# Optimization experiments

Hardware: AMD Instinct MI355X
Metric: run time of the kernel (lower is better)

The kernel has to match this reference:

```python
import jax, jax.numpy as jnp
import numpy as np
from jax import lax

N_STATES = 512
VOCAB = 32000
BATCH = 16
SEQ_LEN = 128


def setup_inputs() -> dict:
    key = jax.random.key(0)
    k_ids, k_em, k_tm, k_p = jax.random.split(key, 4)
    input_ids = jax.random.randint(k_ids, (BATCH, SEQ_LEN), 0, VOCAB, dtype=jnp.int64)
    em = jax.random.normal(k_em, (N_STATES, VOCAB), dtype=jnp.float32)
    tm = jax.random.normal(k_tm, (N_STATES, N_STATES), dtype=jnp.float32)
    p = jax.random.normal(k_p, (N_STATES,), dtype=jnp.float32)
    return {"input_ids": input_ids, "em": em, "tm": tm, "p": p}


def reference(input_ids, em, tm, p):
    """HMM forward algorithm in log space; returns mean NLL (scalar).

    em: [S, V] emission logits, tm: [S, S] transition logits, p: [S] prior logits.
    do_log_softmax=True -> normalize each in log space first.
    """
    log_em = jax.nn.log_softmax(em, axis=-1)   # [S, V]
    log_tm = jax.nn.log_softmax(tm, axis=-1)   # [S, S] rows = source state
    log_p = jax.nn.log_softmax(p, axis=-1)     # [S]

    # Gather emission log-probs per token: [B, T, S]
    em_tok = log_em.T[input_ids]

    # alpha_0[b, s] = log_p[s] + log_em[s, x_0]
    alpha0 = log_p[None, :] + em_tok[:, 0]     # [B, S]

    def step(alpha, e_t):
        # alpha: [B, S_src]; log-matmul: logsumexp over source states
        a = jax.nn.logsumexp(alpha[:, :, None] + log_tm[None, :, :], axis=1) + e_t
        return a, None

    em_rest = jnp.swapaxes(em_tok[:, 1:], 0, 1)  # [T-1, B, S]
    alpha_T, _ = lax.scan(step, alpha0, em_rest)

    # loss = -mean_b log p(x_b) = -mean_b logsumexp_s alpha_T[b, s]
    loss = -jnp.mean(jax.nn.logsumexp(alpha_T, axis=-1))
    return loss
```

## Files before the change

### kernel.cpp

```cpp
#include <hip/hip_runtime.h>
#include <hip/hip_bf16.h>

#define NS 512
#define NV 32000
#define NB 16
#define NT 128

#ifndef __has_builtin
#define __has_builtin(x) 0
#endif

typedef int v8i __attribute__((ext_vector_type(8)));
typedef float v4f __attribute__((ext_vector_type(4)));

__device__ inline unsigned enc_e4m3(float x) {
    x = fminf(x, 448.0f);
    unsigned u = __float_as_uint(x);
    if (x < 0.015625f) {
        return (unsigned)(int)rintf(x * 512.0f);
    }
    unsigned u2 = u + 0x7FFFFu + ((u >> 20) & 1u);
    return (((u2 >> 23) - 120u) << 3) | ((u2 >> 20) & 7u);
}

__device__ inline unsigned pack4_e4m3(float a, float b, float c, float d) {
#if __has_builtin(__builtin_amdgcn_cvt_pk_fp8_f32)
    int v = __builtin_amdgcn_cvt_pk_fp8_f32(a, b, 0, false);
    v = __builtin_amdgcn_cvt_pk_fp8_f32(c, d, v, true);
    return (unsigned)v;
#else
    return enc_e4m3(a) | (enc_e4m3(b) << 8) | (enc_e4m3(c) << 16) | (enc_e4m3(d) << 24);
#endif
}

#define DPPMAX(x, ctrl) \
    x = fmaxf(x, __int_as_float(__builtin_amdgcn_mov_dpp(__float_as_int(x), ctrl, 0xF, 0xF, true)))
#define DPPADD(x, ctrl) \
    x = x + __int_as_float(__builtin_amdgcn_mov_dpp(__float_as_int(x), ctrl, 0xF, 0xF, true))

__global__ __launch_bounds__(256) void k_emtok_T(
    const float* __restrict__ em, const int* __restrict__ ids,
    float* __restrict__ em_lin_T)
{
    const int s   = blockIdx.x;
    const int tid = threadIdx.x;
    const float* row = em + (size_t)s * NV;

    int idv[8];
#pragma unroll
    for (int k = 0; k < 8; ++k) idv[k] = ids[tid + 256 * k];
    float g[8];
#pragma unroll
    for (int k = 0; k < 8; ++k) g[k] = row[idv[k]];

    float sum = 0.f;
    const float4* row4 = (const float4*)row;
#pragma unroll 4
    for (int i = 0; i < 31; ++i) {
        float4 v = row4[tid + 256 * i];
        sum += __expf(v.x) + __expf(v.y) + __expf(v.z) + __expf(v.w);
    }
    sum += __expf(row[31744 + tid]);

#pragma unroll
    for (int off = 32; off; off >>= 1) sum += __shfl_down(sum, off);
    __shared__ float red[4];
    __shared__ float s_scale;
    if ((tid & 63) == 0) red[tid >> 6] = sum;
    __syncthreads();
    if (tid == 0) s_scale = (1.0f / ((red[0] + red[1]) + (red[2] + red[3]))) * 0x1p-18f;
    __syncthreads();
    const float scale = s_scale;

#pragma unroll
    for (int k = 0; k < 8; ++k)
        em_lin_T[(size_t)s * (NB * NT) + tid + 256 * k] = __expf(g[k]) * scale;
}

__global__ __launch_bounds__(256) void k_tr(
    const float* __restrict__ emT, float* __restrict__ em_lin)
{
    __shared__ float tile[32][33];
    const int jb = blockIdx.x * 32;
    const int sb = blockIdx.y * 32;
    const int cc = threadIdx.x & 31;
    const int rr = threadIdx.x >> 5;
#pragma unroll
    for (int i = 0; i < 4; ++i) {
        int r = rr + 8 * i;
        tile[r][cc] = emT[(size_t)(sb + r) * (NB * NT) + jb + cc];
    }
    __syncthreads();
#pragma unroll
    for (int i = 0; i < 4; ++i) {
        int r = rr + 8 * i;
        em_lin[(size_t)(jb + r) * NS + sb + cc] = tile[cc][r];
    }
}

__global__ __launch_bounds__(64) void k_z(
    const float* __restrict__ tm, float* __restrict__ zscale)
{
    const int k    = blockIdx.x;
    const int lane = threadIdx.x;
    const float* row = tm + (size_t)k * NS;

    float4 a = ((const float4*)row)[lane * 2];
    float4 b = ((const float4*)row)[lane * 2 + 1];
    float sum = ((__expf(a.x) + __expf(a.y)) + (__expf(a.z) + __expf(a.w)))
              + ((__expf(b.x) + __expf(b.y)) + (__expf(b.z) + __expf(b.w)));
#pragma unroll
    for (int off = 32; off; off >>= 1) sum += __shfl_down(sum, off);
    if (lane == 0) zscale[k] = 1024.0f / sum;
}

__global__ __launch_bounds__(256) void k_pt2(
    const float* __restrict__ tm, const float* __restrict__ zscale,
    unsigned char* __restrict__ PT)
{
    __shared__ float tile[64][65];
    __shared__ float zs[64];
    const int kb  = blockIdx.x * 64;
    const int db  = blockIdx.y * 64;
    const int tid = threadIdx.x;
    const int c   = tid & 63;
    const int r0  = tid >> 6;

    if (tid < 64) zs[tid] = zscale[kb + tid];
#pragma unroll
    for (int i = 0; i < 16; ++i) {
        int r = r0 + 4 * i;
        tile[r][c] = tm[(size_t)(kb + r) * NS + db + c];
    }
    __syncthreads();

    const int d  = tid >> 2;
    const int ks = (tid & 3) * 16;
    unsigned px[4];
#pragma unroll
    for (int gq = 0; gq < 4; ++gq) {
        int k0 = ks + gq * 4;
        px[gq] = pack4_e4m3(__expf(tile[k0 + 0][d]) * zs[k0 + 0],
                            __expf(tile[k0 + 1][d]) * zs[k0 + 1],
                            __expf(tile[k0 + 2][d]) * zs[k0 + 2],
                            __expf(tile[k0 + 3][d]) * zs[k0 + 3]);
    }
    uint4 o; o.x = px[0]; o.y = px[1]; o.z = px[2]; o.w = px[3];
    *(uint4*)(PT + (size_t)(db + d) * NS + kb + ks) = o;
}

__global__ __launch_bounds__(512, 2) void k_scan(
    const float* __restrict__ em_lin, const unsigned char* __restrict__ PT,
    const float* __restrict__ p, float* __restrict__ out)
{
    const int bb  = blockIdx.x;
    const int tid = threadIdx.x;
    const int w   = tid >> 6;
    const int l   = tid & 63;
    const int lc  = l & 15;
    const int lq  = l >> 4;

    __shared__ unsigned Ew[16 * 128];
    __shared__ unsigned wmE[8][4];
    __shared__ unsigned mbuf[4];
    __shared__ float    wm2[8][4];
    __shared__ float    sbuf[4];

    v8i B[4][4];
#pragma unroll
    for (int nt = 0; nt < 4; ++nt) {
#pragma unroll
        for (int kt = 0; kt < 4; ++kt) {
            const uint4* src = (const uint4*)(PT + (size_t)((w * 4 + nt) * 16 + lc) * NS + kt * 128 + lq * 32);
            uint4 lo = src[0], hi = src[1];
            v8i bb8;
            bb8[0] = (int)lo.x; bb8[1] = (int)lo.y; bb8[2] = (int)lo.z; bb8[3] = (int)lo.w;
            bb8[4] = (int)hi.x; bb8[5] = (int)hi.y; bb8[6] = (int)hi.z; bb8[7] = (int)hi.w;
            B[nt][kt] = bb8;
        }
    }

    float zp = 0.f;
#pragma unroll
    for (int i = 0; i < 8; ++i) zp += __expf(p[l * 8 + i]);
    DPPADD(zp, 0x128); DPPADD(zp, 0x124); DPPADD(zp, 0xB1); DPPADD(zp, 0x4E);
    float Zp = __int_as_float(__builtin_amdgcn_readlane(__float_as_int(zp), 0))
             + __int_as_float(__builtin_amdgcn_readlane(__float_as_int(zp), 16))
             + __int_as_float(__builtin_amdgcn_readlane(__float_as_int(zp), 32))
             + __int_as_float(__builtin_amdgcn_readlane(__float_as_int(zp), 48));
    const float invZp = 1.0f / Zp;

    const int dbase0 = w * 64 + lc;
    const int gb     = bb * 4 + lq;

    const float* epb0 = em_lin + (size_t)gb * (NT * NS) + dbase0;
    float alpha[4];
#pragma unroll
    for (int nt = 0; nt < 4; ++nt)
        alpha[nt] = __expf(p[dbase0 + 16 * nt]) * invZp * epb0[16 * nt];

    int gsum = 18;
    const unsigned sel1 = (l & 1) ? 0x07030501u : 0x02060004u;
    const unsigned sel2 = (l & 2) ? 0x07060302u : 0x01000504u;
    const int mrow = 4 * lq + (l & 3);

    int aidx[8];
#pragma unroll
    for (int kt = 0; kt < 4; ++kt) {
#pragma unroll
        for (int c = 0; c < 2; ++c)
            aidx[kt * 2 + c] = lc * 32 + (((kt * 8 + lq * 2 + c) ^ lc) & 31);
    }
    int widx[4];
#pragma unroll
    for (int nt = 0; nt < 4; ++nt)
        widx[nt] = mrow * 128 + ((((w * 4 + nt) ^ mrow) & 31) << 2) + (lc >> 2);

    const float* epb = epb0 + NS;

    for (int t = 1; t < NT; ++t) {
        float epf[4];
#pragma unroll
        for (int nt = 0; nt < 4; ++nt) epf[nt] = epb[16 * nt];
        epb += NS;

        float mx = fmaxf(fmaxf(alpha[0], alpha[1]), fmaxf(alpha[2], alpha[3]));
        DPPMAX(mx, 0x128); DPPMAX(mx, 0x124); DPPMAX(mx, 0xB1); DPPMAX(mx, 0x4E);
        if (lc == 0) wmE[w][lq] = __float_as_uint(mx) >> 23;
        __syncthreads();

        if (tid < 4) {
            unsigned e0 = wmE[0][tid], e1 = wmE[1][tid], e2 = wmE[2][tid], e3 = wmE[3][tid];
            unsigned e4 = wmE[4][tid], e5 = wmE[5][tid], e6 = wmE[6][tid], e7 = wmE[7][tid];
            unsigned m01 = e0 > e1 ? e0 : e1,  m23 = e2 > e3 ? e2 : e3;
            unsigned m45 = e4 > e5 ? e4 : e5,  m67 = e6 > e7 ? e6 : e7;
            unsigned ma = m01 > m23 ? m01 : m23, mb = m45 > m67 ? m45 : m67;
            mbuf[tid] = ma > mb ? ma : mb;
        }
        __syncthreads();

        const unsigned eb = mbuf[lq];
        const float sc = __uint_as_float((261u - eb) << 23);
        gsum += (int)eb - 126;

#pragma unroll
        for (int nt = 0; nt < 4; ++nt) {
            unsigned dw = pack4_e4m3(alpha[nt] * sc, 0.f, 0.f, 0.f);
            int tmp = __builtin_amdgcn_mov_dpp((int)dw, 0xB1, 0xF, 0xF, true);
            dw = __builtin_amdgcn_perm(dw, (unsigned)tmp, sel1);
            tmp = __builtin_amdgcn_mov_dpp((int)dw, 0x4E, 0xF, 0xF, true);
            dw = __builtin_amdgcn_perm(dw, (unsigned)tmp, sel2);
            Ew[widx[nt]] = dw;
        }
        __syncthreads();

        v8i A[4];
        const uint4* eb4 = (const uint4*)&Ew[0];
#pragma unroll
        for (int kt = 0; kt < 4; ++kt) {
            uint4 lo = eb4[aidx[kt * 2 + 0]];
            uint4 hi = eb4[aidx[kt * 2 + 1]];
            v8i aa;
            aa[0] = (int)lo.x; aa[1] = (int)lo.y; aa[2] = (int)lo.z; aa[3] = (int)lo.w;
            aa[4] = (int)hi.x; aa[5] = (int)hi.y; aa[6] = (int)hi.z; aa[7] = (int)hi.w;
            A[kt] = aa;
        }

        v4f C[4];
#pragma unroll
        for (int nt = 0; nt < 4; ++nt) { C[nt][0] = 0.f; C[nt][1] = 0.f; C[nt][2] = 0.f; C[nt][3] = 0.f; }
#pragma unroll
        for (int kt = 0; kt < 4; ++kt)
#pragma unroll
            for (int nt = 0; nt < 4; ++nt)
                C[nt] = __builtin_amdgcn_mfma_scale_f32_16x16x128_f8f6f4(
                            A[kt], B[nt][kt], C[nt], 0, 0, 0, 0x7F7F7F7F, 0, 0x7F7F7F7F);

#pragma unroll
        for (int nt = 0; nt < 4; ++nt)
            alpha[nt] = C[nt][0] * epf[nt];
    }

    {
        float sm = (alpha[0] + alpha[1]) + (alpha[2] + alpha[3]);
        DPPADD(sm, 0x128); DPPADD(sm, 0x124); DPPADD(sm, 0xB1); DPPADD(sm, 0x4E);
        if (lc == 0) wm2[w][lq] = sm;
        if (w == 0 && lc == 0) sbuf[lq] = (float)gsum;
    }
    __syncthreads();
    if (tid < 4) {
        float s8 = ((wm2[0][tid] + wm2[1][tid]) + (wm2[2][tid] + wm2[3][tid]))
                 + ((wm2[4][tid] + wm2[5][tid]) + (wm2[6][tid] + wm2[7][tid]));
        float L2 = __log2f(s8) + sbuf[tid];
        atomicAdd(out, -(0.693147180559945f / 16.0f) * L2);
    }
}

extern "C" void kernel_launch(void* const* d_in, const int* in_sizes, int n_in,
                              void* d_out, int out_size, void* d_ws, size_t ws_size,
                              hipStream_t stream)
{
    const int*   ids = (const int*)d_in[0];
    const float* em  = (const float*)d_in[1];
    const float* tm  = (const float*)d_in[2];
    const float* p   = (const float*)d_in[3];
    float* out = (float*)d_out;

    float*          em_lin = (float*)d_ws;
    unsigned char*  PT     = (unsigned char*)d_ws + ((size_t)4 << 20);
    float*          zscale = (float*)((unsigned char*)d_ws + ((size_t)4 << 20) + ((size_t)256 << 10));
    float*          emT    = (float*)((unsigned char*)d_ws + ((size_t)4 << 20) + ((size_t)512 << 10));

    hipMemsetAsync(d_out, 0, sizeof(float), stream);

    k_emtok_T<<<NS, 256, 0, stream>>>(em, ids, emT);
    k_tr<<<dim3(64, 16), 256, 0, stream>>>(emT, em_lin);
    k_z<<<NS, 64, 0, stream>>>(tm, zscale);
    k_pt2<<<dim3(8, 8), 256, 0, stream>>>(tm, zscale, PT);
    k_scan<<<4, 512, 0, stream>>>(em_lin, PT, p, out);
}
```

Before: 245.9 us.

## Use per-wave exponents with MFMA block scales to drop two barriers per step

Each wave now quantizes its alpha slice with its own exponent rather than waiting for a block-wide max. The per-wave exponents go into shared memory alongside the FP8 tile, and every lane rebuilds the global max and feeds the relative exponents as MFMA A-operand block scales. The Ew buffer is double-buffered so one barrier per timestep is enough, down from three. The cost is extra per-lane integer work to decode the scales, and a risk of accuracy problems if the scale-lane mapping or the clamping is wrong.

```diff
diff --git a/kernel.cpp b/kernel.cpp
--- a/kernel.cpp
+++ b/kernel.cpp
@@ -38,6 +38,8 @@
 #define DPPADD(x, ctrl) \
     x = x + __int_as_float(__builtin_amdgcn_mov_dpp(__float_as_int(x), ctrl, 0xF, 0xF, true))
 
+#define UMX(a, b) ((a) > (b) ? (a) : (b))
+
 __global__ __launch_bounds__(256) void k_emtok_T(
     const float* __restrict__ em, const int* __restrict__ ids,
     float* __restrict__ em_lin_T)
@@ -160,9 +162,8 @@
     const int lc  = l & 15;
     const int lq  = l >> 4;
 
-    __shared__ unsigned Ew[16 * 128];
-    __shared__ unsigned wmE[8][4];
-    __shared__ unsigned mbuf[4];
+    __shared__ unsigned Ew[2][16 * 128];
+    __shared__ __align__(16) unsigned char wmE[2][32];
     __shared__ float    wm2[8][4];
     __shared__ float    sbuf[4];
 
@@ -216,9 +217,17 @@
     for (int nt = 0; nt < 4; ++nt)
         widx[nt] = mrow * 128 + ((((w * 4 + nt) ^ mrow) & 31) << 2) + (lc >> 2);
 
+    const int bA = lc >> 2;
+    const int h  = lq >> 1;
+    const unsigned shA = (unsigned)(bA << 3);
+    const unsigned shQ = (unsigned)(lq << 3);
+
     const float* epb = epb0 + NS;
 
     for (int t = 1; t < NT; ++t) {
+        const int buf = t & 1;
+        unsigned* EwB = &Ew[buf][0];
+
         float epf[4];
 #pragma unroll
         for (int nt = 0; nt < 4; ++nt) epf[nt] = epb[16 * nt];
@@ -226,22 +235,9 @@
 
         float mx = fmaxf(fmaxf(alpha[0], alpha[1]), fmaxf(alpha[2], alpha[3]));
         DPPMAX(mx, 0x128); DPPMAX(mx, 0x124); DPPMAX(mx, 0xB1); DPPMAX(mx, 0x4E);
-        if (lc == 0) wmE[w][lq] = __float_as_uint(mx) >> 23;
-        __syncthreads();
-
-        if (tid < 4) {
-            unsigned e0 = wmE[0][tid], e1 = wmE[1][tid], e2 = wmE[2][tid], e3 = wmE[3][tid];
-            unsigned e4 = wmE[4][tid], e5 = wmE[5][tid], e6 = wmE[6][tid], e7 = wmE[7][tid];
-            unsigned m01 = e0 > e1 ? e0 : e1,  m23 = e2 > e3 ? e2 : e3;
-            unsigned m45 = e4 > e5 ? e4 : e5,  m67 = e6 > e7 ? e6 : e7;
-            unsigned ma = m01 > m23 ? m01 : m23, mb = m45 > m67 ? m45 : m67;
-            mbuf[tid] = ma > mb ? ma : mb;
-        }
-        __syncthreads();
-
-        const unsigned eb = mbuf[lq];
-        const float sc = __uint_as_float((261u - eb) << 23);
-        gsum += (int)eb - 126;
+        unsigned E = __float_as_uint(mx) >> 23;
+        E = E > 1u ? E : 1u;
+        const float sc = __uint_as_float((261u - E) << 23);
 
 #pragma unroll
         for (int nt = 0; nt < 4; ++nt) {
@@ -250,12 +246,44 @@
             dw = __builtin_amdgcn_perm(dw, (unsigned)tmp, sel1);
             tmp = __builtin_amdgcn_mov_dpp((int)dw, 0x4E, 0xF, 0xF, true);
             dw = __builtin_amdgcn_perm(dw, (unsigned)tmp, sel2);
-            Ew[widx[nt]] = dw;
+            EwB[widx[nt]] = dw;
         }
+        if (lc == 0) wmE[buf][w * 4 + lq] = (unsigned char)E;
         __syncthreads();
 
+        const uint4 ua = *(const uint4*)&wmE[buf][0];
+        const uint4 ub = *(const uint4*)&wmE[buf][16];
+        const unsigned d0 = ua.x, d1 = ua.y, d2 = ua.z, d3 = ua.w;
+        const unsigned d4 = ub.x, d5 = ub.y, d6 = ub.z, d7 = ub.w;
+
+        const unsigned a0 = (d0 >> shA) & 255u, a1 = (d1 >> shA) & 255u;
+        const unsigned a2 = (d2 >> shA) & 255u, a3 = (d3 >> shA) & 255u;
+        const unsigned a4 = (d4 >> shA) & 255u, a5 = (d5 >> shA) & 255u;
+        const unsigned a6 = (d6 >> shA) & 255u, a7 = (d7 >> shA) & 255u;
+        const unsigned MA = UMX(UMX(UMX(a0, a1), UMX(a2, a3)),
+                                UMX(UMX(a4, a5), UMX(a6, a7)));
+
+        const unsigned q0 = (d0 >> shQ) & 255u, q1 = (d1 >> shQ) & 255u;
+        const unsigned q2 = (d2 >> shQ) & 255u, q3 = (d3 >> shQ) & 255u;
+        const unsigned q4 = (d4 >> shQ) & 255u, q5 = (d5 >> shQ) & 255u;
+        const unsigned q6 = (d6 >> shQ) & 255u, q7 = (d7 >> shQ) & 255u;
+        const unsigned MQ = UMX(UMX(UMX(q0, q1), UMX(q2, q3)),
+                                UMX(UMX(q4, q5), UMX(q6, q7)));
+        gsum += (int)MQ - 126;
+
+        const unsigned e0 = h ? a1 : a0;
+        const unsigned e1 = h ? a3 : a2;
+        const unsigned e2 = h ? a5 : a4;
+        const unsigned e3 = h ? a7 : a6;
+        int s0 = (int)e0 + 127 - (int)MA; s0 = s0 < 0 ? 0 : s0;
+        int s1 = (int)e1 + 127 - (int)MA; s1 = s1 < 0 ? 0 : s1;
+        int s2 = (int)e2 + 127 - (int)MA; s2 = s2 < 0 ? 0 : s2;
+        int s3 = (int)e3 + 127 - (int)MA; s3 = s3 < 0 ? 0 : s3;
+        const int scA[4] = { s0 * 0x01010101, s1 * 0x01010101,
+                             s2 * 0x01010101, s3 * 0x01010101 };
+
         v8i A[4];
-        const uint4* eb4 = (const uint4*)&Ew[0];
+        const uint4* eb4 = (const uint4*)EwB;
 #pragma unroll
         for (int kt = 0; kt < 4; ++kt) {
             uint4 lo = eb4[aidx[kt * 2 + 0]];
@@ -274,7 +302,7 @@
 #pragma unroll
             for (int nt = 0; nt < 4; ++nt)
                 C[nt] = __builtin_amdgcn_mfma_scale_f32_16x16x128_f8f6f4(
-                            A[kt], B[nt][kt], C[nt], 0, 0, 0, 0x7F7F7F7F, 0, 0x7F7F7F7F);
+                            A[kt], B[nt][kt], C[nt], 0, 0, 0, scA[kt], 0, 0x7F7F7F7F);
 
 #pragma unroll
         for (int nt = 0; nt < 4; ++nt)
```

After: 244.5 us. About the same (-0.6%).
